# Kernel optimization log

Hardware: AMD Instinct MI355X
Metric: run time of the kernel (lower is better)

The kernel has to match this reference:

```python
import jax, jax.numpy as jnp
import numpy as np

D = 256      # d_model
H = 8        # nhead
HD = D // H  # head_dim
B = 16       # ragged batch size
L = 4096     # tokens per sample (equal lengths here; code handles general ragged)
NQ = 100     # instance queries per sample


def _xavier(key, shape):
    a = float(np.sqrt(6.0 / (shape[0] + shape[1])))
    return jax.random.uniform(key, shape, jnp.float32, -a, a)


def setup_inputs() -> dict:
    key = jax.random.key(0)
    ks = jax.random.split(key, 8)
    total = B * L
    source = jax.random.normal(ks[0], (total, D), jnp.float32)
    query = jax.random.normal(ks[1], (B, NQ, D), jnp.float32)
    batch_offsets = (jnp.arange(B + 1) * L).astype(jnp.int32)
    # nn.MultiheadAttention params: in-proj (split into q/k/v) + out-proj.
    Wq = _xavier(ks[2], (D, D)); bq = jnp.zeros((D,), jnp.float32)
    Wk = _xavier(ks[3], (D, D)); bk = jnp.zeros((D,), jnp.float32)
    Wv = _xavier(ks[4], (D, D)); bv = jnp.zeros((D,), jnp.float32)
    Wo = _xavier(ks[5], (D, D)); bo = jnp.zeros((D,), jnp.float32)
    return {"source": source, "query": query, "batch_offsets": batch_offsets,
            "Wq": Wq, "bq": bq, "Wk": Wk, "bk": bk, "Wv": Wv, "bv": bv,
            "Wo": Wo, "bo": bo}


def reference(source, query, batch_offsets, Wq, bq, Wk, bk, Wv, bv, Wo, bo):
    # Ragged -> padded gather (indices are concrete, computed with numpy).
    offs = np.asarray(batch_offsets)
    lens = offs[1:] - offs[:-1]                      # (B,)
    Lmax = int(lens.max())
    pos = np.arange(Lmax)
    mask = pos[None, :] < lens[:, None]              # (B, Lmax) valid keys
    idx = np.where(mask, offs[:-1, None] + pos[None, :], 0)
    kv_in = source[jnp.asarray(idx)]                 # (B, Lmax, D)

    # Projections (torch Linear: x @ W.T + b), split into heads.
    q = (query @ Wq.T + bq).reshape(B, NQ, H, HD)
    k = (kv_in @ Wk.T + bk).reshape(B, Lmax, H, HD)
    v = (kv_in @ Wv.T + bv).reshape(B, Lmax, H, HD)

    scale = 1.0 / jnp.sqrt(jnp.asarray(HD, q.dtype))
    scores = jnp.einsum("bqhd,bkhd->bhqk", q * scale, k)
    scores = jnp.where(jnp.asarray(mask)[:, None, None, :], scores, -1e30)
    attn = jax.nn.softmax(scores, axis=-1)           # (B, H, NQ, Lmax)
    ctx = jnp.einsum("bhqk,bkhd->bqhd", attn, v).reshape(B, NQ, D)
    out = ctx @ Wo.T + bo
    # Original code: dropout/norm results are discarded; residual add of query.
    return out + query
```

## Files before the change

kernel.cpp:

```cpp
#include <hip/hip_runtime.h>
#include <hip/hip_bf16.h>
#include <math.h>

#define DM     256
#define NHEAD  8
#define HDIM   32
#define QPAD   112
#define NCHUNK 8
#define BM     128
#define BN     128
#define BK     32

typedef __attribute__((ext_vector_type(8))) short bf16x8;
typedef __attribute__((ext_vector_type(4))) short bf16x4;
typedef __attribute__((ext_vector_type(4))) float f32x4;

__device__ __forceinline__ short f2bf(float f) {
  union { float f; unsigned u; } x; x.f = f;
  unsigned u = (x.u + 0x7fffu + ((x.u >> 16) & 1u)) >> 16;
  return (short)u;
}
__device__ __forceinline__ float bf2f(short s) {
  union { unsigned u; float f; } x; x.u = ((unsigned)(unsigned short)s) << 16;
  return x.f;
}
__device__ __forceinline__ bf16x8 bzero8() {
  bf16x8 v;
#pragma unroll
  for (int j = 0; j < 8; j++) v[j] = (short)0;
  return v;
}
__device__ __forceinline__ void gl2lds16(const void* g, void* l) {
  __builtin_amdgcn_global_load_lds(
      (const __attribute__((address_space(1))) unsigned*)g,
      (__attribute__((address_space(3))) unsigned*)l, 16, 0, 0);
}
__device__ __forceinline__ bf16x8 cvt8(const float* p) {
  float4 x0 = *(const float4*)p, x1 = *(const float4*)(p + 4);
  bf16x8 v;
  v[0] = f2bf(x0.x); v[1] = f2bf(x0.y); v[2] = f2bf(x0.z); v[3] = f2bf(x0.w);
  v[4] = f2bf(x1.x); v[5] = f2bf(x1.y); v[6] = f2bf(x1.z); v[7] = f2bf(x1.w);
  return v;
}

__global__ __launch_bounds__(256) void wconv_kernel(
    const float* __restrict__ Wk, const float* __restrict__ Wv,
    short* __restrict__ Wkv) {
  int idx = blockIdx.x * 256 + threadIdx.x;
  int e0 = idx * 8;
  const float* p = (e0 < DM * DM) ? (Wk + e0) : (Wv + (e0 - DM * DM));
  *(bf16x8*)(Wkv + e0) = cvt8(p);
}

__global__ __launch_bounds__(256) void q_proj_kernel(
    const float* __restrict__ query, const float* __restrict__ Wq,
    const float* __restrict__ bq, short* __restrict__ Qw, int Bn, int NQ) {
  int b  = blockIdx.x / (QPAD / 8);
  int r0 = (blockIdx.x % (QPAD / 8)) * 8;
  __shared__ __align__(16) float ql[8 * DM];
  int tid = threadIdx.x;
  for (int i = tid; i < 8 * DM; i += 256) {
    int r = r0 + (i >> 8);
    ql[i] = (r < NQ) ? query[((size_t)b * NQ + r) * DM + (i & 255)] : 0.f;
  }
  __syncthreads();
  int d = tid;
  float bias = bq[d];
  float acc[8];
#pragma unroll
  for (int qi = 0; qi < 8; qi++) acc[qi] = bias;
  const float* wrow = Wq + (size_t)d * DM;
  for (int k = 0; k < DM; k += 4) {
    float4 w = *(const float4*)(wrow + k);
#pragma unroll
    for (int qi = 0; qi < 8; qi++) {
      float4 x = *(const float4*)&ql[qi * DM + k];
      acc[qi] += x.x * w.x + x.y * w.y + x.z * w.z + x.w * w.w;
    }
  }
  const float scale = 0.17677669529663687f;
  int h = d >> 5, hd = d & 31;
#pragma unroll
  for (int qi = 0; qi < 8; qi++) {
    int r = r0 + qi;
    float v = (r < NQ) ? acc[qi] * scale : 0.f;
    Qw[(((size_t)b * NHEAD + h) * QPAD + r) * HDIM + hd] = f2bf(v);
  }
}

__global__ __launch_bounds__(256) void kv_gemm_kernel(
    const float* __restrict__ src, const short* __restrict__ Wkv,
    const float* __restrict__ bk, const float* __restrict__ bv,
    const int* __restrict__ offs, short* __restrict__ Kw,
    short* __restrict__ Vw, int T, int Bn, int Mtiles) {
  int ntile = blockIdx.x / Mtiles;
  int mtile = blockIdx.x % Mtiles;
  int t0 = mtile * BM;
  int n0 = ntile * BN;
  bool isK = (n0 < DM);
  int n0rel = n0 & (DM - 1);
  const float* bias = isK ? bk : bv;

  int tid = threadIdx.x;
  int wave = tid >> 6, lane = tid & 63;
  int l15 = lane & 15, quad = lane >> 4;
  int wm = wave >> 1, wn = wave & 1;

  __shared__ __align__(16) short As[BM][BK + 8];
  __shared__ __align__(16) short Bs[BN * BK];

  f32x4 acc[4][4];
#pragma unroll
  for (int i = 0; i < 4; i++)
#pragma unroll
    for (int j = 0; j < 4; j++) acc[i][j] = (f32x4){0.f, 0.f, 0.f, 0.f};

  for (int kk = 0; kk < DM; kk += BK) {
    __syncthreads();
#pragma unroll
    for (int s2 = 0; s2 < 2; s2++) {
      int s = tid + s2 * 256;
      int row = s >> 2, ch = s & 3;
      int tok = t0 + row;
      if (tok >= T) tok = T - 1;
      *(bf16x8*)&As[row][ch * 8] = cvt8(src + (size_t)tok * DM + kk + ch * 8);
    }
    {
      int cloc = lane >> 2;
#pragma unroll
      for (int j = 0; j < 2; j++) {
        int cb = wave * 32 + j * 16;
        int c = cb + cloc;
        int slot = (lane & 3) ^ ((c >> 1) & 3);
        const short* g = Wkv + (size_t)(n0 + c) * DM + kk + slot * 8;
        gl2lds16(g, &Bs[cb * BK]);
      }
    }
    __syncthreads();
    bf16x8 af[4], bf_[4];
#pragma unroll
    for (int mt = 0; mt < 4; mt++)
      af[mt] = *(const bf16x8*)&As[wm * 64 + mt * 16 + l15][quad * 8];
#pragma unroll
    for (int nt = 0; nt < 4; nt++) {
      int c = wn * 64 + nt * 16 + l15;
      int slot = quad ^ ((c >> 1) & 3);
      bf_[nt] = *(const bf16x8*)&Bs[c * BK + slot * 8];
    }
    if (isK) {
#pragma unroll
      for (int mt = 0; mt < 4; mt++)
#pragma unroll
        for (int nt = 0; nt < 4; nt++)
          acc[mt][nt] = __builtin_amdgcn_mfma_f32_16x16x32_bf16(
              bf_[nt], af[mt], acc[mt][nt], 0, 0, 0);
    } else {
#pragma unroll
      for (int mt = 0; mt < 4; mt++)
#pragma unroll
        for (int nt = 0; nt < 4; nt++)
          acc[mt][nt] = __builtin_amdgcn_mfma_f32_16x16x32_bf16(
              af[mt], bf_[nt], acc[mt][nt], 0, 0, 0);
    }
  }

  if (isK) {
    float bk4[4][4];
    int hK[4], hdK[4];
#pragma unroll
    for (int nt = 0; nt < 4; nt++) {
      int nbq = n0rel + wn * 64 + nt * 16 + quad * 4;
      float4 b4 = *(const float4*)(bias + nbq);
      bk4[nt][0] = b4.x; bk4[nt][1] = b4.y; bk4[nt][2] = b4.z; bk4[nt][3] = b4.w;
      hK[nt] = nbq >> 5;
      hdK[nt] = nbq & 31;
    }
    int bcur = 0;
#pragma unroll
    for (int mt = 0; mt < 4; mt++) {
      int tok = t0 + wm * 64 + mt * 16 + l15;
      if (tok >= T) continue;
      while (bcur + 1 < Bn && offs[bcur + 1] <= tok) bcur++;
      int off = offs[bcur], len = offs[bcur + 1] - off;
      int l = tok - off;
      size_t bb = (size_t)off * DM;
#pragma unroll
      for (int nt = 0; nt < 4; nt++) {
        bf16x4 p;
#pragma unroll
        for (int r = 0; r < 4; r++) p[r] = f2bf(acc[mt][nt][r] + bk4[nt][r]);
        *(bf16x4*)&Kw[bb + (size_t)hK[nt] * len * HDIM + (size_t)l * HDIM +
                      hdK[nt]] = p;
      }
    }
  } else {
    float bV[4];
    int hV[4], hdV[4];
#pragma unroll
    for (int nt = 0; nt < 4; nt++) {
      int nb = n0rel + wn * 64 + nt * 16 + l15;
      bV[nt] = bias[nb];
      hV[nt] = nb >> 5;
      hdV[nt] = nb & 31;
    }
    int bcur = 0;
#pragma unroll
    for (int mt = 0; mt < 4; mt++) {
      int tb = t0 + wm * 64 + mt * 16 + quad * 4;
      if (tb >= T) continue;
      while (bcur + 1 < Bn && offs[bcur + 1] <= tb) bcur++;
      int off = offs[bcur], len = offs[bcur + 1] - off;
      size_t bb = (size_t)off * DM;
      bool span = (tb + 3 < offs[bcur + 1]) && (tb + 3 < T);
      if (span) {
        int l = tb - off;
#pragma unroll
        for (int nt = 0; nt < 4; nt++) {
          size_t idx =
              bb + (size_t)hV[nt] * len * HDIM + (size_t)hdV[nt] * len + l;
          bf16x4 p;
#pragma unroll
          for (int r = 0; r < 4; r++) p[r] = f2bf(acc[mt][nt][r] + bV[nt]);
          if ((idx & 3) == 0) {
            *(bf16x4*)&Vw[idx] = p;
          } else {
#pragma unroll
            for (int r = 0; r < 4; r++) Vw[idx + r] = p[r];
          }
        }
      } else {
        int bc2 = bcur;
#pragma unroll
        for (int r = 0; r < 4; r++) {
          int tok = tb + r;
          if (tok >= T) continue;
          while (bc2 + 1 < Bn && offs[bc2 + 1] <= tok) bc2++;
          int off2 = offs[bc2], len2 = offs[bc2 + 1] - off2;
          int l = tok - off2;
          size_t bb2 = (size_t)off2 * DM;
#pragma unroll
          for (int nt = 0; nt < 4; nt++)
            Vw[bb2 + (size_t)hV[nt] * len2 * HDIM + (size_t)hdV[nt] * len2 +
               l] = f2bf(acc[mt][nt][r] + bV[nt]);
        }
      }
    }
  }
}

__global__ __launch_bounds__(448) void attn_kernel(
    const short* __restrict__ Qw, const short* __restrict__ Kw,
    const short* __restrict__ Vw, const int* __restrict__ offs,
    short* __restrict__ Ops, float* __restrict__ Ml, int Bn) {
  int c  = blockIdx.x % NCHUNK;
  int bh = blockIdx.x / NCHUNK;
  int h = bh % NHEAD, b = bh / NHEAD;
  int wave = threadIdx.x >> 6, lane = threadIdx.x & 63;
  int l15 = lane & 15, quad = lane >> 4;

  int off = offs[b], len = offs[b + 1] - off;
  int cl = ((len + NCHUNK * 32 - 1) / (NCHUNK * 32)) * 32;
  int kstart = c * cl;
  int kend   = min(kstart + cl, len);

  const short* Kh = Kw + (size_t)off * DM + (size_t)h * len * HDIM;
  const short* Vh = Vw + (size_t)off * DM + (size_t)h * len * HDIM;

  int row16 = wave * 16 + l15;
  bf16x8 aq = *(const bf16x8*)(
      Qw + (((size_t)b * NHEAD + h) * QPAD + row16) * HDIM + quad * 8);

  f32x4 o[2];
#pragma unroll
  for (int j = 0; j < 2; j++) o[j] = (f32x4){0.f, 0.f, 0.f, 0.f};
  float mrun[4], lrun[4];
#pragma unroll
  for (int r = 0; r < 4; r++) { mrun[r] = -1e30f; lrun[r] = 0.f; }

  __shared__ __align__(16) short plds[7][16][40];

  for (int kb = kstart; kb < kend; kb += 32) {
    bool valid[2];
    bf16x8 bk_[2];
#pragma unroll
    for (int nt = 0; nt < 2; nt++) {
      int key = kb + nt * 16 + l15;
      valid[nt] = key < kend;
      bk_[nt] = valid[nt]
                    ? *(const bf16x8*)(Kh + (size_t)key * HDIM + quad * 8)
                    : bzero8();
    }
    f32x4 zero = {0.f, 0.f, 0.f, 0.f};
    f32x4 s[2];
#pragma unroll
    for (int nt = 0; nt < 2; nt++)
      s[nt] = __builtin_amdgcn_mfma_f32_16x16x32_bf16(aq, bk_[nt], zero, 0, 0, 0);
#pragma unroll
    for (int r = 0; r < 4; r++) {
      float v0 = valid[0] ? s[0][r] : -1e30f;
      float v1 = valid[1] ? s[1][r] : -1e30f;
      float t = fmaxf(v0, v1);
      t = fmaxf(t, __shfl_xor(t, 1, 16));
      t = fmaxf(t, __shfl_xor(t, 2, 16));
      t = fmaxf(t, __shfl_xor(t, 4, 16));
      t = fmaxf(t, __shfl_xor(t, 8, 16));
      float mn = fmaxf(mrun[r], t);
      float al = __expf(mrun[r] - mn);
      float p0 = valid[0] ? __expf(v0 - mn) : 0.f;
      float p1 = valid[1] ? __expf(v1 - mn) : 0.f;
      float rs = p0 + p1;
      rs += __shfl_xor(rs, 1, 16);
      rs += __shfl_xor(rs, 2, 16);
      rs += __shfl_xor(rs, 4, 16);
      rs += __shfl_xor(rs, 8, 16);
      lrun[r] = al * lrun[r] + rs;
      mrun[r] = mn;
      o[0][r] *= al;
      o[1][r] *= al;
      plds[wave][quad * 4 + r][l15]      = f2bf(p0);
      plds[wave][quad * 4 + r][16 + l15] = f2bf(p1);
    }
    bf16x8 pa = *(const bf16x8*)&plds[wave][l15][quad * 8];
    bf16x8 bv_[2];
#pragma unroll
    for (int ht = 0; ht < 2; ht++) {
      int hd = ht * 16 + l15;
      int k0 = kb + quad * 8;
      const short* p = Vh + (size_t)hd * len + k0;
      if (k0 + 7 < len) {
        bv_[ht] = *(const bf16x8*)p;
      } else {
        bf16x8 v;
#pragma unroll
        for (int j = 0; j < 8; j++) v[j] = (k0 + j < len) ? p[j] : (short)0;
        bv_[ht] = v;
      }
    }
#pragma unroll
    for (int ht = 0; ht < 2; ht++)
      o[ht] = __builtin_amdgcn_mfma_f32_16x16x32_bf16(pa, bv_[ht], o[ht], 0, 0, 0);
  }

#pragma unroll
  for (int r = 0; r < 4; r++) {
    int row = wave * 16 + quad * 4 + r;
    size_t base = (((size_t)c * Bn + b) * NHEAD + h) * QPAD + row;
#pragma unroll
    for (int ht = 0; ht < 2; ht++)
      Ops[base * HDIM + ht * 16 + l15] = f2bf(o[ht][r]);
    if (l15 == 0) {
      Ml[base * 2]     = mrun[r];
      Ml[base * 2 + 1] = lrun[r];
    }
  }
}

__global__ __launch_bounds__(256) void combine_kernel(
    const short* __restrict__ Ops, const float* __restrict__ Ml,
    const float* __restrict__ query, const float* __restrict__ Wo,
    const float* __restrict__ bo, float* __restrict__ out, int Bn, int NQ) {
  int bpb = (NQ + 7) / 8;
  int b  = blockIdx.x / bpb;
  int q0 = (blockIdx.x % bpb) * 8;
  __shared__ __align__(16) float ctx[8 * DM];
  int d = threadIdx.x;
  int h = d >> 5, hd = d & 31;
#pragma unroll
  for (int qi = 0; qi < 8; qi++) {
    int q = q0 + qi;
    float val = 0.f;
    if (q < NQ) {
      float mc[NCHUNK], lc[NCHUNK], M = -1e30f;
#pragma unroll
      for (int c = 0; c < NCHUNK; c++) {
        size_t base = (((size_t)c * Bn + b) * NHEAD + h) * QPAD + q;
        mc[c] = Ml[base * 2];
        lc[c] = Ml[base * 2 + 1];
        M = fmaxf(M, mc[c]);
      }
      float L = 0.f, acc = 0.f;
#pragma unroll
      for (int c = 0; c < NCHUNK; c++) {
        size_t base = (((size_t)c * Bn + b) * NHEAD + h) * QPAD + q;
        float w = __expf(mc[c] - M);
        L += lc[c] * w;
        acc += w * bf2f(Ops[base * HDIM + hd]);
      }
      val = (L > 0.f) ? acc / L : 0.f;
    }
    ctx[qi * DM + d] = val;
  }
  __syncthreads();
  const float* wrow = Wo + (size_t)d * DM;
  float acc[8];
  float bias = bo[d];
#pragma unroll
  for (int qi = 0; qi < 8; qi++) acc[qi] = bias;
  for (int k = 0; k < DM; k += 4) {
    float4 w = *(const float4*)(wrow + k);
#pragma unroll
    for (int qi = 0; qi < 8; qi++) {
      float4 x = *(const float4*)&ctx[qi * DM + k];
      acc[qi] += x.x * w.x + x.y * w.y + x.z * w.z + x.w * w.w;
    }
  }
#pragma unroll
  for (int qi = 0; qi < 8; qi++) {
    int q = q0 + qi;
    if (q < NQ)
      out[((size_t)b * NQ + q) * DM + d] =
          acc[qi] + query[((size_t)b * NQ + q) * DM + d];
  }
}

extern "C" void kernel_launch(void* const* d_in, const int* in_sizes, int n_in,
                              void* d_out, int out_size, void* d_ws,
                              size_t ws_size, hipStream_t stream) {
  const float* src   = (const float*)d_in[0];
  const float* query = (const float*)d_in[1];
  const int*   offs  = (const int*)d_in[2];
  const float* Wq = (const float*)d_in[3];
  const float* bq = (const float*)d_in[4];
  const float* Wk = (const float*)d_in[5];
  const float* bk = (const float*)d_in[6];
  const float* Wv = (const float*)d_in[7];
  const float* bv = (const float*)d_in[8];
  const float* Wo = (const float*)d_in[9];
  const float* bo = (const float*)d_in[10];
  float* out = (float*)d_out;

  int T  = in_sizes[0] / DM;
  int Bn = in_sizes[2] - 1;
  int NQ = in_sizes[1] / (Bn * DM);

  char* w = (char*)d_ws;
  size_t qsz = (size_t)Bn * NHEAD * QPAD * HDIM * 2;
  size_t ksz = (size_t)T * DM * 2;
  size_t osz = (size_t)NCHUNK * Bn * NHEAD * QPAD * HDIM * 2;
  size_t msz = (size_t)NCHUNK * Bn * NHEAD * QPAD * 2 * 4;
  short* Qw  = (short*)w;
  short* Kw  = (short*)(w + qsz);
  short* Vw  = (short*)(w + qsz + ksz);
  short* Ops = (short*)(w + qsz + 2 * ksz);
  float* Mlp = (float*)(w + qsz + 2 * ksz + osz);
  short* Wkv = (short*)(w + qsz + 2 * ksz + osz + msz);

  int Mtiles = (T + BM - 1) / BM;

  wconv_kernel<<<(2 * DM * DM) / (256 * 8), 256, 0, stream>>>(Wk, Wv, Wkv);
  q_proj_kernel<<<Bn * (QPAD / 8), 256, 0, stream>>>(query, Wq, bq, Qw, Bn, NQ);
  kv_gemm_kernel<<<Mtiles * (2 * DM / BN), 256, 0, stream>>>(
      src, Wkv, bk, bv, offs, Kw, Vw, T, Bn, Mtiles);
  attn_kernel<<<Bn * NHEAD * NCHUNK, 448, 0, stream>>>(Qw, Kw, Vw, offs, Ops,
                                                       Mlp, Bn);
  combine_kernel<<<Bn * ((NQ + 7) / 8), 256, 0, stream>>>(Ops, Mlp, query, Wo,
                                                          bo, out, Bn, NQ);
}
```

Baseline: 271.4 us.

## Double-buffer KV GEMM tiles with prefetch and reshape tiles to 64x256

```diff
diff --git a/kernel.cpp b/kernel.cpp
--- a/kernel.cpp
+++ b/kernel.cpp
@@ -7,8 +7,8 @@
 #define HDIM   32
 #define QPAD   112
 #define NCHUNK 8
-#define BM     128
-#define BN     128
+#define BM     64
+#define BN     256
 #define BK     32
 
 typedef __attribute__((ext_vector_type(8))) short bf16x8;
@@ -37,6 +37,12 @@
 }
 __device__ __forceinline__ bf16x8 cvt8(const float* p) {
   float4 x0 = *(const float4*)p, x1 = *(const float4*)(p + 4);
+  bf16x8 v;
+  v[0] = f2bf(x0.x); v[1] = f2bf(x0.y); v[2] = f2bf(x0.z); v[3] = f2bf(x0.w);
+  v[4] = f2bf(x1.x); v[5] = f2bf(x1.y); v[6] = f2bf(x1.z); v[7] = f2bf(x1.w);
+  return v;
+}
+__device__ __forceinline__ bf16x8 pack8(float4 x0, float4 x1) {
   bf16x8 v;
   v[0] = f2bf(x0.x); v[1] = f2bf(x0.y); v[2] = f2bf(x0.z); v[3] = f2bf(x0.w);
   v[4] = f2bf(x1.x); v[5] = f2bf(x1.y); v[6] = f2bf(x1.z); v[7] = f2bf(x1.w);
@@ -93,21 +99,21 @@
     const float* __restrict__ bk, const float* __restrict__ bv,
     const int* __restrict__ offs, short* __restrict__ Kw,
     short* __restrict__ Vw, int T, int Bn, int Mtiles) {
-  int ntile = blockIdx.x / Mtiles;
-  int mtile = blockIdx.x % Mtiles;
+  int bid = blockIdx.x;
+  int mtile = (bid >> 4) * 8 + (bid & 7);
+  int ntile = (bid >> 3) & 1;
+  if (mtile >= Mtiles) return;
   int t0 = mtile * BM;
   int n0 = ntile * BN;
-  bool isK = (n0 < DM);
-  int n0rel = n0 & (DM - 1);
+  bool isK = (ntile == 0);
   const float* bias = isK ? bk : bv;
 
   int tid = threadIdx.x;
   int wave = tid >> 6, lane = tid & 63;
   int l15 = lane & 15, quad = lane >> 4;
-  int wm = wave >> 1, wn = wave & 1;
-
-  __shared__ __align__(16) short As[BM][BK + 8];
-  __shared__ __align__(16) short Bs[BN * BK];
+
+  __shared__ __align__(16) short As[2][BM][BK + 8];
+  __shared__ __align__(16) short Bs[2][BN * BK];
 
   f32x4 acc[4][4];
 #pragma unroll
@@ -115,37 +121,50 @@
 #pragma unroll
     for (int j = 0; j < 4; j++) acc[i][j] = (f32x4){0.f, 0.f, 0.f, 0.f};
 
-  for (int kk = 0; kk < DM; kk += BK) {
-    __syncthreads();
-#pragma unroll
-    for (int s2 = 0; s2 < 2; s2++) {
-      int s = tid + s2 * 256;
-      int row = s >> 2, ch = s & 3;
-      int tok = t0 + row;
-      if (tok >= T) tok = T - 1;
-      *(bf16x8*)&As[row][ch * 8] = cvt8(src + (size_t)tok * DM + kk + ch * 8);
-    }
-    {
-      int cloc = lane >> 2;
-#pragma unroll
-      for (int j = 0; j < 2; j++) {
-        int cb = wave * 32 + j * 16;
-        int c = cb + cloc;
-        int slot = (lane & 3) ^ ((c >> 1) & 3);
-        const short* g = Wkv + (size_t)(n0 + c) * DM + kk + slot * 8;
-        gl2lds16(g, &Bs[cb * BK]);
-      }
-    }
-    __syncthreads();
+  int arow = tid >> 2, ach = tid & 3;
+  int atok = t0 + arow;
+  if (atok >= T) atok = T - 1;
+  const float* asrc = src + (size_t)atok * DM + ach * 8;
+
+#define STAGE_B(buf, kk)                                                   \
+  {                                                                        \
+    int cloc = lane >> 2;                                                  \
+    for (int j = 0; j < 4; j++) {                                          \
+      int cb = wave * 64 + j * 16;          \
+      int c = cb + cloc;                   \
+      int slot = (lane & 3) ^ ((c >> 1) & 3);                              \
+      const short* g = Wkv + (size_t)(n0 + c) * DM + (kk) + slot * 8;      \
+      gl2lds16(g, &Bs[buf][cb * BK]);                                      \
+    }                                                                      \
+  }
+
+  {
+    float4 a0 = *(const float4*)asrc;
+    float4 a1 = *(const float4*)(asrc + 4);
+    STAGE_B(0, 0);
+    *(bf16x8*)&As[0][arow][ach * 8] = pack8(a0, a1);
+  }
+  __syncthreads();
+
+  for (int ki = 0; ki < DM / BK; ki++) {
+    int cur = ki & 1;
+    bool more = (ki + 1 < DM / BK);
+    float4 na0, na1;
+    if (more) {
+      const float* ap = asrc + (ki + 1) * BK;
+      na0 = *(const float4*)ap;
+      na1 = *(const float4*)(ap + 4);
+      STAGE_B(cur ^ 1, (ki + 1) * BK);
+    }
     bf16x8 af[4], bf_[4];
 #pragma unroll
     for (int mt = 0; mt < 4; mt++)
-      af[mt] = *(const bf16x8*)&As[wm * 64 + mt * 16 + l15][quad * 8];
+      af[mt] = *(const bf16x8*)&As[cur][mt * 16 + l15][quad * 8];
 #pragma unroll
     for (int nt = 0; nt < 4; nt++) {
-      int c = wn * 64 + nt * 16 + l15;
+      int c = wave * 64 + nt * 16 + l15;
       int slot = quad ^ ((c >> 1) & 3);
-      bf_[nt] = *(const bf16x8*)&Bs[c * BK + slot * 8];
+      bf_[nt] = *(const bf16x8*)&Bs[cur][c * BK + slot * 8];
     }
     if (isK) {
 #pragma unroll
@@ -162,14 +181,18 @@
           acc[mt][nt] = __builtin_amdgcn_mfma_f32_16x16x32_bf16(
               af[mt], bf_[nt], acc[mt][nt], 0, 0, 0);
     }
-  }
+    if (more)
+      *(bf16x8*)&As[cur ^ 1][arow][ach * 8] = pack8(na0, na1);
+    __syncthreads();
+  }
+#undef STAGE_B
 
   if (isK) {
     float bk4[4][4];
     int hK[4], hdK[4];
 #pragma unroll
     for (int nt = 0; nt < 4; nt++) {
-      int nbq = n0rel + wn * 64 + nt * 16 + quad * 4;
+      int nbq = wave * 64 + nt * 16 + quad * 4;
       float4 b4 = *(const float4*)(bias + nbq);
       bk4[nt][0] = b4.x; bk4[nt][1] = b4.y; bk4[nt][2] = b4.z; bk4[nt][3] = b4.w;
       hK[nt] = nbq >> 5;
@@ -178,7 +201,7 @@
     int bcur = 0;
 #pragma unroll
     for (int mt = 0; mt < 4; mt++) {
-      int tok = t0 + wm * 64 + mt * 16 + l15;
+      int tok = t0 + mt * 16 + l15;
       if (tok >= T) continue;
       while (bcur + 1 < Bn && offs[bcur + 1] <= tok) bcur++;
       int off = offs[bcur], len = offs[bcur + 1] - off;
@@ -198,7 +221,7 @@
     int hV[4], hdV[4];
 #pragma unroll
     for (int nt = 0; nt < 4; nt++) {
-      int nb = n0rel + wn * 64 + nt * 16 + l15;
+      int nb = wave * 64 + nt * 16 + l15;
       bV[nt] = bias[nb];
       hV[nt] = nb >> 5;
       hdV[nt] = nb & 31;
@@ -206,7 +229,7 @@
     int bcur = 0;
 #pragma unroll
     for (int mt = 0; mt < 4; mt++) {
-      int tb = t0 + wm * 64 + mt * 16 + quad * 4;
+      int tb = t0 + mt * 16 + quad * 4;
       if (tb >= T) continue;
       while (bcur + 1 < Bn && offs[bcur + 1] <= tb) bcur++;
       int off = offs[bcur], len = offs[bcur + 1] - off;
@@ -446,10 +469,11 @@
   short* Wkv = (short*)(w + qsz + 2 * ksz + osz + msz);
 
   int Mtiles = (T + BM - 1) / BM;
+  int groups = (Mtiles + 7) / 8;
 
   wconv_kernel<<<(2 * DM * DM) / (256 * 8), 256, 0, stream>>>(Wk, Wv, Wkv);
   q_proj_kernel<<<Bn * (QPAD / 8), 256, 0, stream>>>(query, Wq, bq, Qw, Bn, NQ);
-  kv_gemm_kernel<<<Mtiles * (2 * DM / BN), 256, 0, stream>>>(
+  kv_gemm_kernel<<<groups * 16, 256, 0, stream>>>(
       src, Wkv, bk, bv, offs, Kw, Vw, T, Bn, Mtiles);
   attn_kernel<<<Bn * NHEAD * NCHUNK, 448, 0, stream>>>(Qw, Kw, Vw, offs, Ops,
                                                        Mlp, Bn);
```

After: 299.7 us. 10.4% more time.

## Retile KV GEMM to 64x256 blocks with grouped K/V tile scheduling

Applied to the files above, without the earlier changes.

```diff
diff --git a/kernel.cpp b/kernel.cpp
--- a/kernel.cpp
+++ b/kernel.cpp
@@ -7,8 +7,8 @@
 #define HDIM   32
 #define QPAD   112
 #define NCHUNK 8
-#define BM     128
-#define BN     128
+#define BM     64
+#define BN     256
 #define BK     32
 
 typedef __attribute__((ext_vector_type(8))) short bf16x8;
@@ -93,18 +93,18 @@
     const float* __restrict__ bk, const float* __restrict__ bv,
     const int* __restrict__ offs, short* __restrict__ Kw,
     short* __restrict__ Vw, int T, int Bn, int Mtiles) {
-  int ntile = blockIdx.x / Mtiles;
-  int mtile = blockIdx.x % Mtiles;
+  int bid = blockIdx.x;
+  int mtile = (bid >> 4) * 8 + (bid & 7);
+  int ntile = (bid >> 3) & 1;
+  if (mtile >= Mtiles) return;
   int t0 = mtile * BM;
   int n0 = ntile * BN;
-  bool isK = (n0 < DM);
-  int n0rel = n0 & (DM - 1);
+  bool isK = (ntile == 0);
   const float* bias = isK ? bk : bv;
 
   int tid = threadIdx.x;
   int wave = tid >> 6, lane = tid & 63;
   int l15 = lane & 15, quad = lane >> 4;
-  int wm = wave >> 1, wn = wave & 1;
 
   __shared__ __align__(16) short As[BM][BK + 8];
   __shared__ __align__(16) short Bs[BN * BK];
@@ -115,21 +115,19 @@
 #pragma unroll
     for (int j = 0; j < 4; j++) acc[i][j] = (f32x4){0.f, 0.f, 0.f, 0.f};
 
+  int arow = tid >> 2, ach = tid & 3;
+  int atok = t0 + arow;
+  if (atok >= T) atok = T - 1;
+  const float* asrc = src + (size_t)atok * DM + ach * 8;
+
   for (int kk = 0; kk < DM; kk += BK) {
     __syncthreads();
-#pragma unroll
-    for (int s2 = 0; s2 < 2; s2++) {
-      int s = tid + s2 * 256;
-      int row = s >> 2, ch = s & 3;
-      int tok = t0 + row;
-      if (tok >= T) tok = T - 1;
-      *(bf16x8*)&As[row][ch * 8] = cvt8(src + (size_t)tok * DM + kk + ch * 8);
-    }
+    *(bf16x8*)&As[arow][ach * 8] = cvt8(asrc + kk);
     {
       int cloc = lane >> 2;
 #pragma unroll
-      for (int j = 0; j < 2; j++) {
-        int cb = wave * 32 + j * 16;
+      for (int j = 0; j < 4; j++) {
+        int cb = wave * 64 + j * 16;
         int c = cb + cloc;
         int slot = (lane & 3) ^ ((c >> 1) & 3);
         const short* g = Wkv + (size_t)(n0 + c) * DM + kk + slot * 8;
@@ -140,10 +138,10 @@
     bf16x8 af[4], bf_[4];
 #pragma unroll
     for (int mt = 0; mt < 4; mt++)
-      af[mt] = *(const bf16x8*)&As[wm * 64 + mt * 16 + l15][quad * 8];
+      af[mt] = *(const bf16x8*)&As[mt * 16 + l15][quad * 8];
 #pragma unroll
     for (int nt = 0; nt < 4; nt++) {
-      int c = wn * 64 + nt * 16 + l15;
+      int c = wave * 64 + nt * 16 + l15;
       int slot = quad ^ ((c >> 1) & 3);
       bf_[nt] = *(const bf16x8*)&Bs[c * BK + slot * 8];
     }
@@ -169,7 +167,7 @@
     int hK[4], hdK[4];
 #pragma unroll
     for (int nt = 0; nt < 4; nt++) {
-      int nbq = n0rel + wn * 64 + nt * 16 + quad * 4;
+      int nbq = wave * 64 + nt * 16 + quad * 4;
       float4 b4 = *(const float4*)(bias + nbq);
       bk4[nt][0] = b4.x; bk4[nt][1] = b4.y; bk4[nt][2] = b4.z; bk4[nt][3] = b4.w;
       hK[nt] = nbq >> 5;
@@ -178,7 +176,7 @@
     int bcur = 0;
 #pragma unroll
     for (int mt = 0; mt < 4; mt++) {
-      int tok = t0 + wm * 64 + mt * 16 + l15;
+      int tok = t0 + mt * 16 + l15;
       if (tok >= T) continue;
       while (bcur + 1 < Bn && offs[bcur + 1] <= tok) bcur++;
       int off = offs[bcur], len = offs[bcur + 1] - off;
@@ -198,7 +196,7 @@
     int hV[4], hdV[4];
 #pragma unroll
     for (int nt = 0; nt < 4; nt++) {
-      int nb = n0rel + wn * 64 + nt * 16 + l15;
+      int nb = wave * 64 + nt * 16 + l15;
       bV[nt] = bias[nb];
       hV[nt] = nb >> 5;
       hdV[nt] = nb & 31;
@@ -206,7 +204,7 @@
     int bcur = 0;
 #pragma unroll
     for (int mt = 0; mt < 4; mt++) {
-      int tb = t0 + wm * 64 + mt * 16 + quad * 4;
+      int tb = t0 + mt * 16 + quad * 4;
       if (tb >= T) continue;
       while (bcur + 1 < Bn && offs[bcur + 1] <= tb) bcur++;
       int off = offs[bcur], len = offs[bcur + 1] - off;
@@ -446,10 +444,11 @@
   short* Wkv = (short*)(w + qsz + 2 * ksz + osz + msz);
 
   int Mtiles = (T + BM - 1) / BM;
+  int groups = (Mtiles + 7) / 8;
 
   wconv_kernel<<<(2 * DM * DM) / (256 * 8), 256, 0, stream>>>(Wk, Wv, Wkv);
   q_proj_kernel<<<Bn * (QPAD / 8), 256, 0, stream>>>(query, Wq, bq, Qw, Bn, NQ);
-  kv_gemm_kernel<<<Mtiles * (2 * DM / BN), 256, 0, stream>>>(
+  kv_gemm_kernel<<<groups * 16, 256, 0, stream>>>(
       src, Wkv, bk, bv, offs, Kw, Vw, T, Bn, Mtiles);
   attn_kernel<<<Bn * NHEAD * NCHUNK, 448, 0, stream>>>(Qw, Kw, Vw, offs, Ops,
                                                        Mlp, Bn);
```

Measured after the change: 273.9 us. No clear change (+0.9%).
